# Optimization experiments

Measured on AMD Instinct MI355X. Metric: run time of the kernel, lower is better.

Reference implementation:

```python
import jax, jax.numpy as jnp
import numpy as np

B, D, L = 2, 256, 512
NL, DS, DC = 2, 16, 4  # n_layers per direction, d_state, d_conv (mamba defaults, expand=2)


def _group_params(key, dm, n):
    di = 2 * dm                 # d_inner = expand * d_model
    r = -(-dm // 16)            # dt_rank = ceil(d_model / 16)
    ks = jax.random.split(key, 6)
    return dict(
        in_w=jax.random.normal(ks[0], (n, 2 * di, dm)) * 0.02,
        conv_w=jax.random.normal(ks[1], (n, di, DC)) * 0.1,
        conv_b=jnp.zeros((n, di)),
        xproj_w=jax.random.normal(ks[2], (n, r + 2 * DS, di)) * 0.02,
        dt_w=jax.random.normal(ks[3], (n, di, r)) * 0.02,
        dt_b=jax.random.normal(ks[4], (n, di)) * 0.02,
        A_log=jnp.log(jnp.tile(jnp.arange(1, DS + 1, dtype=jnp.float32), (n, di, 1))),
        D=jnp.ones((n, di)),
        out_w=jax.random.normal(ks[5], (n, dm, di)) * 0.02,
    )


def setup_inputs() -> dict:
    key = jax.random.key(0)
    kx, ka, kb = jax.random.split(key, 3)
    inp = {"x": jax.random.normal(kx, (B, D, L), dtype=jnp.float32)}
    # group a: seq-direction mambas (d_model = L); group b: channel-direction (d_model = D)
    for pfx, dm, k in (("a_", L, ka), ("b_", D, kb)):
        for name, v in _group_params(k, dm, NL).items():
            inp[pfx + name] = v
    return inp


def _mamba_layer(x, in_w, conv_w, conv_b, xproj_w, dt_w, dt_b, A_log, Dp, out_w):
    b, l, dm = x.shape
    di = in_w.shape[0] // 2
    r = dt_w.shape[1]
    xz = jnp.einsum('bld,ed->ble', x, in_w)            # (b,l,2*di)
    xi, z = jnp.split(xz, 2, axis=-1)
    # causal depthwise conv along the sequence dim
    xc = jax.lax.conv_general_dilated(
        xi.transpose(0, 2, 1), conv_w[:, None, :], (1,), [(DC - 1, 0)],
        feature_group_count=di, dimension_numbers=('NCH', 'OIH', 'NCH'))
    xi = jax.nn.silu((xc + conv_b[None, :, None]).transpose(0, 2, 1))   # (b,l,di)
    x_dbl = jnp.einsum('bld,ed->ble', xi, xproj_w)
    dt, Bm, Cm = jnp.split(x_dbl, [r, r + DS], axis=-1)
    dt = jax.nn.softplus(jnp.einsum('blr,dr->bld', dt, dt_w) + dt_b)    # (b,l,di)
    A = -jnp.exp(A_log)                                                 # (di,DS)
    dA = jnp.exp(dt[..., None] * A)                                     # (b,l,di,DS)
    dBu = dt[..., None] * Bm[:, :, None, :] * xi[..., None]             # (b,l,di,DS)

    def step(h, inp):
        dA_t, dBu_t, C_t = inp
        h = dA_t * h + dBu_t
        return h, jnp.einsum('bds,bs->bd', h, C_t)

    h0 = jnp.zeros((b, di, DS), x.dtype)
    _, ys = jax.lax.scan(step, h0, (dA.transpose(1, 0, 2, 3),
                                    dBu.transpose(1, 0, 2, 3),
                                    Cm.transpose(1, 0, 2)))
    y = ys.transpose(1, 0, 2) + Dp * xi
    y = y * jax.nn.silu(z)
    return jnp.einsum('bld,od->blo', y, out_w)


def _stack(x, p):
    for k in range(NL):
        x = _mamba_layer(x, p['in_w'][k], p['conv_w'][k], p['conv_b'][k],
                         p['xproj_w'][k], p['dt_w'][k], p['dt_b'][k],
                         p['A_log'][k], p['D'][k], p['out_w'][k])
    return x


def reference(x, a_in_w, a_conv_w, a_conv_b, a_xproj_w, a_dt_w, a_dt_b, a_A_log, a_D, a_out_w,
              b_in_w, b_conv_w, b_conv_b, b_xproj_w, b_dt_w, b_dt_b, b_A_log, b_D, b_out_w):
    pa = dict(in_w=a_in_w, conv_w=a_conv_w, conv_b=a_conv_b, xproj_w=a_xproj_w,
              dt_w=a_dt_w, dt_b=a_dt_b, A_log=a_A_log, D=a_D, out_w=a_out_w)
    pb = dict(in_w=b_in_w, conv_w=b_conv_w, conv_b=b_conv_b, xproj_w=b_xproj_w,
              dt_w=b_dt_w, dt_b=b_dt_b, A_log=b_A_log, D=b_D, out_w=b_out_w)
    h = _stack(x, pa)                                        # mamba over last dim L on (B,D,L)
    h = _stack(h.transpose(0, 2, 1), pb).transpose(0, 2, 1)  # mamba over channel dim D
    return x + h
```

## Files before the change

kernel.cpp:

```cpp
#include <hip/hip_runtime.h>
#include <cstdint>

typedef float f32x4 __attribute__((ext_vector_type(4)));
typedef __bf16 bf16x8 __attribute__((ext_vector_type(8)));
typedef __bf16 bf16x4 __attribute__((ext_vector_type(4)));

#define SCAN_TC 32

struct CvtP {
    const float* cs[5]; __bf16* cd[5]; int cn[5]; int nvec;
    const float* xpb; __bf16* xpb_d;
};

__global__ __launch_bounds__(256)
void cvt_all(CvtP p)
{
    const int idx = blockIdx.x * 256 + threadIdx.x;
    if (idx < p.nvec) {
        int off = idx * 4, sgm = 0;
        while (off >= p.cn[sgm]) { off -= p.cn[sgm]; ++sgm; }
        f32x4 v = *(const f32x4*)(p.cs[sgm] + off);
        bf16x4 o;
#pragma unroll
        for (int j = 0; j < 4; ++j) o[j] = (__bf16)v[j];
        *(bf16x4*)(p.cd[sgm] + off) = o;
    } else {
        const int i = idx - p.nvec;
        if (i < 2 * 64 * 512) {
            const int c = i & 511, r = (i >> 9) & 63, l = i >> 15;
            float v = (r < 48) ? p.xpb[((size_t)l * 48 + r) * 512 + c] : 0.f;
            p.xpb_d[i] = (__bf16)v;
        }
    }
}

__global__ __launch_bounds__(256)
void gemm_f32A(const float* __restrict__ A, const __bf16* __restrict__ W,
               float* __restrict__ C, int M, int N, int K)
{
    __shared__ __bf16 sA[64 * 64];
    __shared__ __bf16 sW[64 * 64];
    const int tid = threadIdx.x;
    const int bm = blockIdx.y * 64, bn = blockIdx.x * 64;
    const int lane = tid & 63, wv = tid >> 6;
    const int m_off = (wv & 1) * 32, n_off = (wv >> 1) * 32;
    const int fr = lane & 15, fq = lane >> 4;
    f32x4 acc[2][2] = {};

    for (int k0 = 0; k0 < K; k0 += 64) {
#pragma unroll
        for (int i = 0; i < 2; ++i) {
            const int cid = i * 256 + tid;
            const int row = cid >> 3, kc = cid & 7;
            const int slot = kc ^ (row & 7);
            const float* sa = A + (size_t)(bm + row) * K + k0 + kc * 8;
            f32x4 v0 = *(const f32x4*)sa;
            f32x4 v1 = *(const f32x4*)(sa + 4);
            bf16x8 ab;
#pragma unroll
            for (int j = 0; j < 4; ++j) { ab[j] = (__bf16)v0[j]; ab[4 + j] = (__bf16)v1[j]; }
            *(bf16x8*)&sA[row * 64 + slot * 8] = ab;
            *(bf16x8*)&sW[row * 64 + slot * 8] =
                *(const bf16x8*)(W + (size_t)(bn + row) * K + k0 + kc * 8);
        }
        __syncthreads();
#pragma unroll
        for (int ks = 0; ks < 2; ++ks) {
            const int kc = ks * 4 + fq;
            const int r0 = m_off + fr, r1 = m_off + 16 + fr;
            const int c0 = n_off + fr, c1 = n_off + 16 + fr;
            bf16x8 a0 = *(const bf16x8*)&sA[r0 * 64 + (kc ^ (r0 & 7)) * 8];
            bf16x8 a1 = *(const bf16x8*)&sA[r1 * 64 + (kc ^ (r1 & 7)) * 8];
            bf16x8 b0 = *(const bf16x8*)&sW[c0 * 64 + (kc ^ (c0 & 7)) * 8];
            bf16x8 b1 = *(const bf16x8*)&sW[c1 * 64 + (kc ^ (c1 & 7)) * 8];
            acc[0][0] = __builtin_amdgcn_mfma_f32_16x16x32_bf16(a0, b0, acc[0][0], 0, 0, 0);
            acc[0][1] = __builtin_amdgcn_mfma_f32_16x16x32_bf16(a0, b1, acc[0][1], 0, 0, 0);
            acc[1][0] = __builtin_amdgcn_mfma_f32_16x16x32_bf16(a1, b0, acc[1][0], 0, 0, 0);
            acc[1][1] = __builtin_amdgcn_mfma_f32_16x16x32_bf16(a1, b1, acc[1][1], 0, 0, 0);
        }
        __syncthreads();
    }
#pragma unroll
    for (int i = 0; i < 2; ++i)
#pragma unroll
        for (int j = 0; j < 2; ++j)
#pragma unroll
            for (int r = 0; r < 4; ++r)
                C[(size_t)(bm + m_off + i * 16 + fq * 4 + r) * N
                  + bn + n_off + j * 16 + fr] = acc[i][j][r];
}

__global__ __launch_bounds__(256)
void gemm_b16A(const __bf16* __restrict__ A, const __bf16* __restrict__ W,
               float* __restrict__ C, int M, int N, int K)
{
    __shared__ __bf16 sA[64 * 64];
    __shared__ __bf16 sW[64 * 64];
    const int tid = threadIdx.x;
    const int bm = blockIdx.y * 64, bn = blockIdx.x * 64;
    const int lane = tid & 63, wv = tid >> 6;
    const int m_off = (wv & 1) * 32, n_off = (wv >> 1) * 32;
    const int fr = lane & 15, fq = lane >> 4;
    f32x4 acc[2][2] = {};

    for (int k0 = 0; k0 < K; k0 += 64) {
#pragma unroll
        for (int i = 0; i < 2; ++i) {
            const int cid = i * 256 + tid;
            const int row = cid >> 3, kc = cid & 7;
            const int slot = kc ^ (row & 7);
            *(bf16x8*)&sA[row * 64 + slot * 8] =
                *(const bf16x8*)(A + (size_t)(bm + row) * K + k0 + kc * 8);
            *(bf16x8*)&sW[row * 64 + slot * 8] =
                *(const bf16x8*)(W + (size_t)(bn + row) * K + k0 + kc * 8);
        }
        __syncthreads();
#pragma unroll
        for (int ks = 0; ks < 2; ++ks) {
            const int kc = ks * 4 + fq;
            const int r0 = m_off + fr, r1 = m_off + 16 + fr;
            const int c0 = n_off + fr, c1 = n_off + 16 + fr;
            bf16x8 a0 = *(const bf16x8*)&sA[r0 * 64 + (kc ^ (r0 & 7)) * 8];
            bf16x8 a1 = *(const bf16x8*)&sA[r1 * 64 + (kc ^ (r1 & 7)) * 8];
            bf16x8 b0 = *(const bf16x8*)&sW[c0 * 64 + (kc ^ (c0 & 7)) * 8];
            bf16x8 b1 = *(const bf16x8*)&sW[c1 * 64 + (kc ^ (c1 & 7)) * 8];
            acc[0][0] = __builtin_amdgcn_mfma_f32_16x16x32_bf16(a0, b0, acc[0][0], 0, 0, 0);
            acc[0][1] = __builtin_amdgcn_mfma_f32_16x16x32_bf16(a0, b1, acc[0][1], 0, 0, 0);
            acc[1][0] = __builtin_amdgcn_mfma_f32_16x16x32_bf16(a1, b0, acc[1][0], 0, 0, 0);
            acc[1][1] = __builtin_amdgcn_mfma_f32_16x16x32_bf16(a1, b1, acc[1][1], 0, 0, 0);
        }
        __syncthreads();
    }
#pragma unroll
    for (int i = 0; i < 2; ++i)
#pragma unroll
        for (int j = 0; j < 2; ++j)
#pragma unroll
            for (int r = 0; r < 4; ++r)
                C[(size_t)(bm + m_off + i * 16 + fq * 4 + r) * N
                  + bn + n_off + j * 16 + fr] = acc[i][j][r];
}

__global__ __launch_bounds__(256)
void gemm_out(const __bf16* __restrict__ A, const __bf16* __restrict__ W,
              void* __restrict__ dst, const float* __restrict__ resid,
              int M, int N, int K, int Lb, int mode)
{
    const int tid = threadIdx.x, lane = tid & 63, wv = tid >> 6;
    const int bm = blockIdx.y * 32 + (wv & 1) * 16;
    const int bn = blockIdx.x * 32 + (wv >> 1) * 16;
    const int fr = lane & 15, fq = lane >> 4;
    const __bf16* arow = A + (size_t)(bm + fr) * K + fq * 8;
    const __bf16* brow = W + (size_t)(bn + fr) * K + fq * 8;
    f32x4 acc0 = {}, acc1 = {};
#pragma unroll 2
    for (int k0 = 0; k0 < K; k0 += 64) {
        bf16x8 a0 = *(const bf16x8*)(arow + k0);
        bf16x8 b0 = *(const bf16x8*)(brow + k0);
        bf16x8 a1 = *(const bf16x8*)(arow + k0 + 32);
        bf16x8 b1 = *(const bf16x8*)(brow + k0 + 32);
        acc0 = __builtin_amdgcn_mfma_f32_16x16x32_bf16(a0, b0, acc0, 0, 0, 0);
        acc1 = __builtin_amdgcn_mfma_f32_16x16x32_bf16(a1, b1, acc1, 0, 0, 0);
    }
    f32x4 acc = acc0 + acc1;
    const int col = bn + fr;
#pragma unroll
    for (int r = 0; r < 4; ++r) {
        const int gm = bm + fq * 4 + r;
        if (mode == 0) {
            ((__bf16*)dst)[(size_t)gm * N + col] = (__bf16)acc[r];
        } else {
            const int b = gm / Lb, t = gm - b * Lb;
            const size_t o = ((size_t)(b * N + col)) * Lb + t;
            if (mode == 1) ((__bf16*)dst)[o] = (__bf16)acc[r];
            else ((float*)dst)[o] = acc[r] + resid[o];
        }
    }
}

__global__ __launch_bounds__(256)
void fused_xp(const float* __restrict__ xz, const float* __restrict__ conv_w,
              const float* __restrict__ conv_b, const __bf16* __restrict__ W,
              float* __restrict__ xi_out, float* __restrict__ pbuf,
              int M, int K, int KC, int Lb)
{
    __shared__ __bf16 sA[64 * 64];
    __shared__ __bf16 sW[64 * 64];
    const int tid = threadIdx.x;
    const int bm = blockIdx.y * 64;
    const int kb = blockIdx.x * KC;
    const int lane = tid & 63, wv = tid >> 6;
    const int m_off = (wv & 1) * 32, n_off = (wv >> 1) * 32;
    const int fr = lane & 15, fq = lane >> 4;
    const int DI = K;
    const int b = bm / Lb;
    const int tbase = bm - b * Lb;
    f32x4 acc[2][2] = {};

    for (int k0 = kb; k0 < kb + KC; k0 += 64) {
#pragma unroll
        for (int i = 0; i < 2; ++i) {
            const int cid = i * 256 + tid;
            const int row = cid >> 3, kc = cid & 7;
            const int slot = kc ^ (row & 7);
            const int d0 = k0 + kc * 8;
            const int t = tbase + row;
            f32x4 a0 = *(const f32x4*)&conv_b[d0];
            f32x4 a1 = *(const f32x4*)&conv_b[d0 + 4];
            f32x4 wc[8];
#pragma unroll
            for (int cch = 0; cch < 8; ++cch)
                wc[cch] = *(const f32x4*)&conv_w[(size_t)(d0 + cch) * 4];
#pragma unroll
            for (int jj = 0; jj < 4; ++jj) {
                const int tt = t - 3 + jj;
                if (tt >= 0) {
                    const float* src = xz + (size_t)(b * Lb + tt) * (2 * DI) + d0;
                    f32x4 v0 = *(const f32x4*)src;
                    f32x4 v1 = *(const f32x4*)(src + 4);
#pragma unroll
                    for (int cch = 0; cch < 4; ++cch) {
                        a0[cch] = fmaf(wc[cch][jj], v0[cch], a0[cch]);
                        a1[cch] = fmaf(wc[4 + cch][jj], v1[cch], a1[cch]);
                    }
                }
            }
            f32x4 r0v, r1v; bf16x8 ab;
#pragma unroll
            for (int cch = 0; cch < 4; ++cch) {
                const float u0 = a0[cch], u1 = a1[cch];
                const float s0 = u0 / (1.f + __expf(-u0));
                const float s1 = u1 / (1.f + __expf(-u1));
                r0v[cch] = s0; r1v[cch] = s1;
                ab[cch] = (__bf16)s0; ab[4 + cch] = (__bf16)s1;
            }
            const size_t mrow = (size_t)(bm + row);
            *(f32x4*)&xi_out[mrow * DI + d0] = r0v;
            *(f32x4*)&xi_out[mrow * DI + d0 + 4] = r1v;
            *(bf16x8*)&sA[row * 64 + slot * 8] = ab;
            *(bf16x8*)&sW[row * 64 + slot * 8] =
                *(const bf16x8*)(W + (size_t)row * K + k0 + kc * 8);
        }
        __syncthreads();
#pragma unroll
        for (int ksu = 0; ksu < 2; ++ksu) {
            const int kc = ksu * 4 + fq;
            const int r0 = m_off + fr, r1 = m_off + 16 + fr;
            const int c0 = n_off + fr, c1 = n_off + 16 + fr;
            bf16x8 a0 = *(const bf16x8*)&sA[r0 * 64 + (kc ^ (r0 & 7)) * 8];
            bf16x8 a1 = *(const bf16x8*)&sA[r1 * 64 + (kc ^ (r1 & 7)) * 8];
            bf16x8 b0 = *(const bf16x8*)&sW[c0 * 64 + (kc ^ (c0 & 7)) * 8];
            bf16x8 b1 = *(const bf16x8*)&sW[c1 * 64 + (kc ^ (c1 & 7)) * 8];
            acc[0][0] = __builtin_amdgcn_mfma_f32_16x16x32_bf16(a0, b0, acc[0][0], 0, 0, 0);
            acc[0][1] = __builtin_amdgcn_mfma_f32_16x16x32_bf16(a0, b1, acc[0][1], 0, 0, 0);
            acc[1][0] = __builtin_amdgcn_mfma_f32_16x16x32_bf16(a1, b0, acc[1][0], 0, 0, 0);
            acc[1][1] = __builtin_amdgcn_mfma_f32_16x16x32_bf16(a1, b1, acc[1][1], 0, 0, 0);
        }
        __syncthreads();
    }
    float* out = pbuf + (size_t)blockIdx.x * M * 64;
#pragma unroll
    for (int i = 0; i < 2; ++i)
#pragma unroll
        for (int jj = 0; jj < 2; ++jj)
#pragma unroll
            for (int r = 0; r < 4; ++r)
                out[(size_t)(bm + m_off + i * 16 + fq * 4 + r) * 64
                    + n_off + jj * 16 + fr] = acc[i][jj][r];
}

__global__ __launch_bounds__(256)
void xp_reduce(const float* __restrict__ pbuf, float* __restrict__ xdbl,
               int total, int KS)
{
    const int idx = (blockIdx.x * 256 + threadIdx.x) * 4;
    if (idx >= total) return;
    f32x4 s = {0.f, 0.f, 0.f, 0.f};
    for (int ks = 0; ks < KS; ++ks)
        s += *(const f32x4*)(pbuf + (size_t)ks * total + idx);
    *(f32x4*)(xdbl + idx) = s;
}

__global__ __launch_bounds__(256)
void scan_p1(const float* __restrict__ xi, const float* __restrict__ xdbl,
             const float* __restrict__ dtw, const float* __restrict__ dtb,
             const float* __restrict__ A_log,
             float* __restrict__ wsA, float* __restrict__ wsB,
             int Bb, int Lb, int DI, int R, int P)
{
    __shared__ float s_xd[SCAN_TC][64];
    __shared__ float s_dt[SCAN_TC][16];
    __shared__ float s_xi[SCAN_TC][16];
    __shared__ float s_w[16 * 33];
    __shared__ float s_db[16];
    const int tid = threadIdx.x;
    const int s = tid & 15, dl = tid >> 4;
    const int nDB = DI / 16;
    const int cpb = P * nDB;
    const int b = blockIdx.x / cpb;
    const int rem = blockIdx.x % cpb;
    const int c = rem / nDB;
    const int d0 = (rem % nDB) * 16;
    const int d = d0 + dl;
    const size_t rowbase = (size_t)b * Lb + (size_t)c * SCAN_TC;

    for (int idx = tid; idx < 16 * R; idx += 256)
        s_w[(idx / R) * 33 + (idx % R)] = dtw[(size_t)(d0 + idx / R) * R + idx % R];
    if (tid < 16) s_db[tid] = dtb[d0 + tid];
#pragma unroll
    for (int i = 0; i < 8; ++i) {
        const int e = i * 256 + tid;
        const int tt = e >> 6, col = e & 63;
        s_xd[tt][col] = xdbl[(rowbase + tt) * 64 + col];
    }
#pragma unroll
    for (int i = 0; i < 2; ++i) {
        const int e = i * 256 + tid;
        const int tt = e >> 4, dd = e & 15;
        s_xi[tt][dd] = xi[(rowbase + tt) * DI + d0 + dd];
    }
    __syncthreads();
#pragma unroll
    for (int i = 0; i < 2; ++i) {
        const int pr = i * 256 + tid;
        const int tt = pr >> 4, dd = pr & 15;
        float v = s_db[dd];
        for (int r = 0; r < R; ++r) v = fmaf(s_xd[tt][r], s_w[dd * 33 + r], v);
        s_dt[tt][dd] = fmaxf(v, 0.f) + log1pf(__expf(-fabsf(v)));
    }
    __syncthreads();
    const float A = -__expf(A_log[(size_t)d * 16 + s]);
    float h = 0.f, sdt = 0.f;
#pragma unroll 4
    for (int t = 0; t < SCAN_TC; ++t) {
        const float dtv = s_dt[t][dl];
        const float xv  = s_xi[t][dl];
        const float Bv  = s_xd[t][R + s];
        h = fmaf(__expf(dtv * A), h, dtv * Bv * xv);
        sdt += dtv;
    }
    const size_t o = ((size_t)(b * P + c) * DI + d) * 16 + s;
    wsA[o] = __expf(sdt * A);
    wsB[o] = h;
}

__global__ __launch_bounds__(256)
void scan_p23(const float* __restrict__ xi, const float* __restrict__ xdbl,
              const float* __restrict__ xz,
              const float* __restrict__ dtw, const float* __restrict__ dtb,
              const float* __restrict__ A_log, const float* __restrict__ Dp,
              const float* __restrict__ wsA, const float* __restrict__ wsB,
              __bf16* __restrict__ y,
              int Bb, int Lb, int DI, int R, int P)
{
    __shared__ float s_xd[SCAN_TC][64];
    __shared__ float s_dt[SCAN_TC][16];
    __shared__ float s_xi[SCAN_TC][16];
    __shared__ float s_z [SCAN_TC][16];
    __shared__ float s_w[16 * 33];
    __shared__ float s_db[16];
    const int tid = threadIdx.x;
    const int s = tid & 15, dl = tid >> 4;
    const int nDB = DI / 16;
    const int cpb = P * nDB;
    const int b = blockIdx.x / cpb;
    const int rem = blockIdx.x % cpb;
    const int c = rem / nDB;
    const int d0 = (rem % nDB) * 16;
    const int d = d0 + dl;
    const size_t rowbase = (size_t)b * Lb + (size_t)c * SCAN_TC;

    for (int idx = tid; idx < 16 * R; idx += 256)
        s_w[(idx / R) * 33 + (idx % R)] = dtw[(size_t)(d0 + idx / R) * R + idx % R];
    if (tid < 16) s_db[tid] = dtb[d0 + tid];
#pragma unroll
    for (int i = 0; i < 8; ++i) {
        const int e = i * 256 + tid;
        const int tt = e >> 6, col = e & 63;
        s_xd[tt][col] = xdbl[(rowbase + tt) * 64 + col];
    }
#pragma unroll
    for (int i = 0; i < 2; ++i) {
        const int e = i * 256 + tid;
        const int tt = e >> 4, dd = e & 15;
        s_xi[tt][dd] = xi[(rowbase + tt) * DI + d0 + dd];
        s_z [tt][dd] = xz[(rowbase + tt) * (size_t)(2 * DI) + DI + d0 + dd];
    }
    __syncthreads();
#pragma unroll
    for (int i = 0; i < 2; ++i) {
        const int pr = i * 256 + tid;
        const int tt = pr >> 4, dd = pr & 15;
        float v = s_db[dd];
        for (int r = 0; r < R; ++r) v = fmaf(s_xd[tt][r], s_w[dd * 33 + r], v);
        s_dt[tt][dd] = fmaxf(v, 0.f) + log1pf(__expf(-fabsf(v)));
    }
    __syncthreads();
    const float A = -__expf(A_log[(size_t)d * 16 + s]);
    const float Dv = Dp[d];

    float h = 0.f;
    for (int cc = 0; cc < c; ++cc) {
        const size_t oc = ((size_t)(b * P + cc) * DI + d) * 16 + s;
        h = fmaf(wsA[oc], h, wsB[oc]);
    }
#pragma unroll 2
    for (int t = 0; t < SCAN_TC; ++t) {
        const float dtv = s_dt[t][dl];
        const float xv  = s_xi[t][dl];
        const float Bv  = s_xd[t][R + s];
        const float Cv  = s_xd[t][R + 16 + s];
        h = fmaf(__expf(dtv * A), h, dtv * Bv * xv);
        float p = h * Cv;
        p += __shfl_xor(p, 1, 16);
        p += __shfl_xor(p, 2, 16);
        p += __shfl_xor(p, 4, 16);
        p += __shfl_xor(p, 8, 16);
        if (s == 0) {
            const float zv = s_z[t][dl];
            const float sig = __fdividef(zv, 1.f + __expf(-zv));
            y[(rowbase + t) * DI + d] = (__bf16)((p + Dv * xv) * sig);
        }
    }
}

extern "C" void kernel_launch(void* const* d_in, const int* in_sizes, int n_in,
                              void* d_out, int out_size, void* d_ws, size_t ws_size,
                              hipStream_t stream)
{
    const float* x       = (const float*)d_in[0];
    const float* a_in_w  = (const float*)d_in[1];
    const float* a_convw = (const float*)d_in[2];
    const float* a_convb = (const float*)d_in[3];
    const float* a_xproj = (const float*)d_in[4];
    const float* a_dtw   = (const float*)d_in[5];
    const float* a_dtb   = (const float*)d_in[6];
    const float* a_Alog  = (const float*)d_in[7];
    const float* a_Dp    = (const float*)d_in[8];
    const float* a_outw  = (const float*)d_in[9];
    const float* b_in_w  = (const float*)d_in[10];
    const float* b_convw = (const float*)d_in[11];
    const float* b_convb = (const float*)d_in[12];
    const float* b_xproj = (const float*)d_in[13];
    const float* b_dtw   = (const float*)d_in[14];
    const float* b_dtb   = (const float*)d_in[15];
    const float* b_Alog  = (const float*)d_in[16];
    const float* b_Dp    = (const float*)d_in[17];
    const float* b_outw  = (const float*)d_in[18];

    float* ws = (float*)d_ws;
    float* buf_xz   = ws;
    float* buf_xi   = buf_xz + 1048576;
    float* buf_xd   = buf_xi + 524288;
    float* buf_pk   = buf_xd + 65536;
    float* buf_wsA  = buf_pk + 524288;
    float* buf_wsB  = buf_wsA + 262144;
    __bf16* wb       = (__bf16*)(buf_wsB + 262144);
    __bf16* wb_a_in  = wb;
    __bf16* wb_a_out = wb_a_in + 2097152;
    __bf16* wb_b_in  = wb_a_out + 1048576;
    __bf16* wb_b_out = wb_b_in + 524288;
    __bf16* wb_xp_a  = wb_b_out + 262144;
    __bf16* wb_xp_b  = wb_xp_a + 131072;
    __bf16* buf_xb   = wb_xp_b + 65536;
    __bf16* buf_x2b  = buf_xb + 262144;
    __bf16* buf_yb   = buf_x2b + 262144;

    {
        CvtP cp;
        cp.cs[0] = a_in_w;  cp.cd[0] = wb_a_in;  cp.cn[0] = 2097152;
        cp.cs[1] = a_outw;  cp.cd[1] = wb_a_out; cp.cn[1] = 1048576;
        cp.cs[2] = b_in_w;  cp.cd[2] = wb_b_in;  cp.cn[2] = 524288;
        cp.cs[3] = b_outw;  cp.cd[3] = wb_b_out; cp.cn[3] = 262144;
        cp.cs[4] = a_xproj; cp.cd[4] = wb_xp_a;  cp.cn[4] = 131072;
        cp.nvec = (2097152 + 1048576 + 524288 + 262144 + 131072) / 4;
        cp.xpb = b_xproj; cp.xpb_d = wb_xp_b;
        const int nthr = cp.nvec + 2 * 64 * 512;
        cvt_all<<<(nthr + 255) / 256, 256, 0, stream>>>(cp);
    }

    for (int k = 0; k < 2; ++k) {
        const int Bb = 2, Lb = 256, DM = 512, DI = 1024, R = 32, P = 8, KS = 16;
        const int M = Bb * Lb;
        if (k == 0)
            gemm_f32A<<<dim3(2 * DI / 64, M / 64), 256, 0, stream>>>(
                x, wb_a_in + (size_t)k * 2 * DI * DM, buf_xz, M, 2 * DI, DM);
        else
            gemm_b16A<<<dim3(2 * DI / 64, M / 64), 256, 0, stream>>>(
                buf_xb, wb_a_in + (size_t)k * 2 * DI * DM, buf_xz, M, 2 * DI, DM);
        fused_xp<<<dim3(KS, M / 64), 256, 0, stream>>>(
            buf_xz, a_convw + (size_t)k * DI * 4, a_convb + (size_t)k * DI,
            wb_xp_a + (size_t)k * 64 * DI, buf_xi, buf_pk, M, DI, DI / KS, Lb);
        xp_reduce<<<(M * 64 / 4 + 255) / 256, 256, 0, stream>>>(
            buf_pk, buf_xd, M * 64, KS);
        scan_p1<<<Bb * P * DI / 16, 256, 0, stream>>>(
            buf_xi, buf_xd, a_dtw + (size_t)k * DI * R, a_dtb + (size_t)k * DI,
            a_Alog + (size_t)k * DI * 16, buf_wsA, buf_wsB, Bb, Lb, DI, R, P);
        scan_p23<<<Bb * P * DI / 16, 256, 0, stream>>>(
            buf_xi, buf_xd, buf_xz, a_dtw + (size_t)k * DI * R, a_dtb + (size_t)k * DI,
            a_Alog + (size_t)k * DI * 16, a_Dp + (size_t)k * DI,
            buf_wsA, buf_wsB, buf_yb, Bb, Lb, DI, R, P);
        if (k == 0)
            gemm_out<<<dim3(DM / 32, M / 32), 256, 0, stream>>>(
                buf_yb, wb_a_out + (size_t)k * DM * DI, buf_xb, nullptr,
                M, DM, DI, Lb, 0);
        else
            gemm_out<<<dim3(DM / 32, M / 32), 256, 0, stream>>>(
                buf_yb, wb_a_out + (size_t)k * DM * DI, buf_x2b, nullptr,
                M, DM, DI, Lb, 1);
    }

    for (int k = 0; k < 2; ++k) {
        const int Bb = 2, Lb = 512, DM = 256, DI = 512, R = 16, P = 16, KS = 8;
        const int M = Bb * Lb;
        const __bf16* src = (k == 0) ? buf_x2b : buf_xb;
        gemm_b16A<<<dim3(2 * DI / 64, M / 64), 256, 0, stream>>>(
            src, wb_b_in + (size_t)k * 2 * DI * DM, buf_xz, M, 2 * DI, DM);
        fused_xp<<<dim3(KS, M / 64), 256, 0, stream>>>(
            buf_xz, b_convw + (size_t)k * DI * 4, b_convb + (size_t)k * DI,
            wb_xp_b + (size_t)k * 64 * DI, buf_xi, buf_pk, M, DI, DI / KS, Lb);
        xp_reduce<<<(M * 64 / 4 + 255) / 256, 256, 0, stream>>>(
            buf_pk, buf_xd, M * 64, KS);
        scan_p1<<<Bb * P * DI / 16, 256, 0, stream>>>(
            buf_xi, buf_xd, b_dtw + (size_t)k * DI * R, b_dtb + (size_t)k * DI,
            b_Alog + (size_t)k * DI * 16, buf_wsA, buf_wsB, Bb, Lb, DI, R, P);
        scan_p23<<<Bb * P * DI / 16, 256, 0, stream>>>(
            buf_xi, buf_xd, buf_xz, b_dtw + (size_t)k * DI * R, b_dtb + (size_t)k * DI,
            b_Alog + (size_t)k * DI * 16, b_Dp + (size_t)k * DI,
            buf_wsA, buf_wsB, buf_yb, Bb, Lb, DI, R, P);
        if (k == 0)
            gemm_out<<<dim3(DM / 32, M / 32), 256, 0, stream>>>(
                buf_yb, wb_b_out + (size_t)k * DM * DI, buf_xb, nullptr,
                M, DM, DI, Lb, 0);
        else
            gemm_out<<<dim3(DM / 32, M / 32), 256, 0, stream>>>(
                buf_yb, wb_b_out + (size_t)k * DM * DI, d_out, x,
                M, DM, DI, Lb, 2);
    }
}
```

Before: 218.9 us.

## Fuse chunked scan passes into one kernel with in-block carry propagation

Replaces the two-kernel chunked selective scan (chunk summaries written to global workspace, then a second kernel that re-reduces all prior chunk summaries serially) with one kernel per (batch, 8-channel group). Each block of 512 threads covers all chunks of the sequence in four chunk groups, keeps chunk summaries in shared memory, runs a short serial prefix over chunks, then recomputes each chunk with its carried state. This removes a launch per layer, the global workspace round trip and the quadratic carry loop. In exchange the grid is much smaller (256 or 128 blocks), each block loops over chunks sequentially, and dt and the x_dbl tiles are recomputed or reloaded in both passes.

```diff
diff --git a/kernel.cpp b/kernel.cpp
--- a/kernel.cpp
+++ b/kernel.cpp
@@ -6,6 +6,7 @@
 typedef __bf16 bf16x4 __attribute__((ext_vector_type(4)));
 
 #define SCAN_TC 32
+#define NG 4
 
 struct CvtP {
     const float* cs[5]; __bf16* cd[5]; int cn[5]; int nvec;
@@ -281,145 +282,123 @@
     *(f32x4*)(xdbl + idx) = s;
 }
 
-__global__ __launch_bounds__(256)
-void scan_p1(const float* __restrict__ xi, const float* __restrict__ xdbl,
-             const float* __restrict__ dtw, const float* __restrict__ dtb,
-             const float* __restrict__ A_log,
-             float* __restrict__ wsA, float* __restrict__ wsB,
-             int Bb, int Lb, int DI, int R, int P)
-{
-    __shared__ float s_xd[SCAN_TC][64];
-    __shared__ float s_dt[SCAN_TC][16];
-    __shared__ float s_xi[SCAN_TC][16];
-    __shared__ float s_w[16 * 33];
-    __shared__ float s_db[16];
+__global__ __launch_bounds__(512)
+void scan_fused(const float* __restrict__ xi, const float* __restrict__ xdbl,
+                const float* __restrict__ xz,
+                const float* __restrict__ dtw, const float* __restrict__ dtb,
+                const float* __restrict__ A_log, const float* __restrict__ Dp,
+                __bf16* __restrict__ y, int Bb, int Lb, int DI, int R, int P)
+{
+    __shared__ float s_xd[NG][SCAN_TC][64];
+    __shared__ float s_xi[NG][SCAN_TC][8];
+    __shared__ float s_z [NG][SCAN_TC][8];
+    __shared__ float s_dt[NG][SCAN_TC][8];
+    __shared__ float s_w[8][33];
+    __shared__ float s_db[8];
+    __shared__ float sumA[16][128];
+    __shared__ float sumB[16][128];
+
     const int tid = threadIdx.x;
-    const int s = tid & 15, dl = tid >> 4;
-    const int nDB = DI / 16;
-    const int cpb = P * nDB;
-    const int b = blockIdx.x / cpb;
-    const int rem = blockIdx.x % cpb;
-    const int c = rem / nDB;
-    const int d0 = (rem % nDB) * 16;
+    const int cg = tid >> 7;
+    const int lt = tid & 127;
+    const int s = lt & 15, dl = lt >> 4;
+    const int nD8 = DI >> 3;
+    const int b = blockIdx.x / nD8;
+    const int d0 = (blockIdx.x % nD8) * 8;
     const int d = d0 + dl;
-    const size_t rowbase = (size_t)b * Lb + (size_t)c * SCAN_TC;
-
-    for (int idx = tid; idx < 16 * R; idx += 256)
-        s_w[(idx / R) * 33 + (idx % R)] = dtw[(size_t)(d0 + idx / R) * R + idx % R];
-    if (tid < 16) s_db[tid] = dtb[d0 + tid];
-#pragma unroll
-    for (int i = 0; i < 8; ++i) {
-        const int e = i * 256 + tid;
-        const int tt = e >> 6, col = e & 63;
-        s_xd[tt][col] = xdbl[(rowbase + tt) * 64 + col];
-    }
-#pragma unroll
-    for (int i = 0; i < 2; ++i) {
-        const int e = i * 256 + tid;
-        const int tt = e >> 4, dd = e & 15;
-        s_xi[tt][dd] = xi[(rowbase + tt) * DI + d0 + dd];
-    }
-    __syncthreads();
-#pragma unroll
-    for (int i = 0; i < 2; ++i) {
-        const int pr = i * 256 + tid;
-        const int tt = pr >> 4, dd = pr & 15;
-        float v = s_db[dd];
-        for (int r = 0; r < R; ++r) v = fmaf(s_xd[tt][r], s_w[dd * 33 + r], v);
-        s_dt[tt][dd] = fmaxf(v, 0.f) + log1pf(__expf(-fabsf(v)));
-    }
-    __syncthreads();
-    const float A = -__expf(A_log[(size_t)d * 16 + s]);
-    float h = 0.f, sdt = 0.f;
-#pragma unroll 4
-    for (int t = 0; t < SCAN_TC; ++t) {
-        const float dtv = s_dt[t][dl];
-        const float xv  = s_xi[t][dl];
-        const float Bv  = s_xd[t][R + s];
-        h = fmaf(__expf(dtv * A), h, dtv * Bv * xv);
-        sdt += dtv;
-    }
-    const size_t o = ((size_t)(b * P + c) * DI + d) * 16 + s;
-    wsA[o] = __expf(sdt * A);
-    wsB[o] = h;
-}
-
-__global__ __launch_bounds__(256)
-void scan_p23(const float* __restrict__ xi, const float* __restrict__ xdbl,
-              const float* __restrict__ xz,
-              const float* __restrict__ dtw, const float* __restrict__ dtb,
-              const float* __restrict__ A_log, const float* __restrict__ Dp,
-              const float* __restrict__ wsA, const float* __restrict__ wsB,
-              __bf16* __restrict__ y,
-              int Bb, int Lb, int DI, int R, int P)
-{
-    __shared__ float s_xd[SCAN_TC][64];
-    __shared__ float s_dt[SCAN_TC][16];
-    __shared__ float s_xi[SCAN_TC][16];
-    __shared__ float s_z [SCAN_TC][16];
-    __shared__ float s_w[16 * 33];
-    __shared__ float s_db[16];
-    const int tid = threadIdx.x;
-    const int s = tid & 15, dl = tid >> 4;
-    const int nDB = DI / 16;
-    const int cpb = P * nDB;
-    const int b = blockIdx.x / cpb;
-    const int rem = blockIdx.x % cpb;
-    const int c = rem / nDB;
-    const int d0 = (rem % nDB) * 16;
-    const int d = d0 + dl;
-    const size_t rowbase = (size_t)b * Lb + (size_t)c * SCAN_TC;
-
-    for (int idx = tid; idx < 16 * R; idx += 256)
-        s_w[(idx / R) * 33 + (idx % R)] = dtw[(size_t)(d0 + idx / R) * R + idx % R];
-    if (tid < 16) s_db[tid] = dtb[d0 + tid];
-#pragma unroll
-    for (int i = 0; i < 8; ++i) {
-        const int e = i * 256 + tid;
-        const int tt = e >> 6, col = e & 63;
-        s_xd[tt][col] = xdbl[(rowbase + tt) * 64 + col];
-    }
-#pragma unroll
-    for (int i = 0; i < 2; ++i) {
-        const int e = i * 256 + tid;
-        const int tt = e >> 4, dd = e & 15;
-        s_xi[tt][dd] = xi[(rowbase + tt) * DI + d0 + dd];
-        s_z [tt][dd] = xz[(rowbase + tt) * (size_t)(2 * DI) + DI + d0 + dd];
-    }
-    __syncthreads();
-#pragma unroll
-    for (int i = 0; i < 2; ++i) {
-        const int pr = i * 256 + tid;
-        const int tt = pr >> 4, dd = pr & 15;
-        float v = s_db[dd];
-        for (int r = 0; r < R; ++r) v = fmaf(s_xd[tt][r], s_w[dd * 33 + r], v);
-        s_dt[tt][dd] = fmaxf(v, 0.f) + log1pf(__expf(-fabsf(v)));
-    }
-    __syncthreads();
+    const int CPG = P / NG;
+
+    for (int idx = tid; idx < 8 * R; idx += 512)
+        s_w[idx / R][idx % R] = dtw[(size_t)(d0 + idx / R) * R + idx % R];
+    if (tid < 8) s_db[tid] = dtb[d0 + tid];
     const float A = -__expf(A_log[(size_t)d * 16 + s]);
     const float Dv = Dp[d];
 
-    float h = 0.f;
-    for (int cc = 0; cc < c; ++cc) {
-        const size_t oc = ((size_t)(b * P + cc) * DI + d) * 16 + s;
-        h = fmaf(wsA[oc], h, wsB[oc]);
-    }
+    for (int i = 0; i < CPG; ++i) {
+        const int c = cg + i * NG;
+        const size_t rowbase = (size_t)b * Lb + (size_t)c * SCAN_TC;
+        __syncthreads();
+        {
+            const f32x4* src = (const f32x4*)(xdbl + rowbase * 64);
+            f32x4* dst = (f32x4*)&s_xd[cg][0][0];
+            for (int e = lt; e < 512; e += 128) dst[e] = src[e];
+        }
+        for (int e = lt; e < 256; e += 128) {
+            const int tt = e >> 3, dd = e & 7;
+            s_xi[cg][tt][dd] = xi[(rowbase + tt) * DI + d0 + dd];
+        }
+        __syncthreads();
+        for (int e = lt; e < 256; e += 128) {
+            const int tt = e >> 3, dd = e & 7;
+            float v = s_db[dd];
+            for (int r = 0; r < R; ++r) v = fmaf(s_xd[cg][tt][r], s_w[dd][r], v);
+            s_dt[cg][tt][dd] = fmaxf(v, 0.f) + log1pf(__expf(-fabsf(v)));
+        }
+        __syncthreads();
+        float h = 0.f, sdt = 0.f;
+#pragma unroll 4
+        for (int t = 0; t < SCAN_TC; ++t) {
+            const float dtv = s_dt[cg][t][dl];
+            const float xv  = s_xi[cg][t][dl];
+            const float Bv  = s_xd[cg][t][R + s];
+            h = fmaf(__expf(dtv * A), h, dtv * Bv * xv);
+            sdt += dtv;
+        }
+        sumA[c][lt] = __expf(sdt * A);
+        sumB[c][lt] = h;
+    }
+    __syncthreads();
+
+    if (tid < 128) {
+        float h = 0.f;
+        for (int c = 0; c < P; ++c) {
+            const float a = sumA[c][tid], bv = sumB[c][tid];
+            sumA[c][tid] = h;
+            h = fmaf(a, h, bv);
+        }
+    }
+    __syncthreads();
+
+    for (int i = 0; i < CPG; ++i) {
+        const int c = cg + i * NG;
+        const size_t rowbase = (size_t)b * Lb + (size_t)c * SCAN_TC;
+        float h = sumA[c][lt];
+        __syncthreads();
+        {
+            const f32x4* src = (const f32x4*)(xdbl + rowbase * 64);
+            f32x4* dst = (f32x4*)&s_xd[cg][0][0];
+            for (int e = lt; e < 512; e += 128) dst[e] = src[e];
+        }
+        for (int e = lt; e < 256; e += 128) {
+            const int tt = e >> 3, dd = e & 7;
+            s_xi[cg][tt][dd] = xi[(rowbase + tt) * DI + d0 + dd];
+            s_z [cg][tt][dd] = xz[(rowbase + tt) * (size_t)(2 * DI) + DI + d0 + dd];
+        }
+        __syncthreads();
+        for (int e = lt; e < 256; e += 128) {
+            const int tt = e >> 3, dd = e & 7;
+            float v = s_db[dd];
+            for (int r = 0; r < R; ++r) v = fmaf(s_xd[cg][tt][r], s_w[dd][r], v);
+            s_dt[cg][tt][dd] = fmaxf(v, 0.f) + log1pf(__expf(-fabsf(v)));
+        }
+        __syncthreads();
 #pragma unroll 2
-    for (int t = 0; t < SCAN_TC; ++t) {
-        const float dtv = s_dt[t][dl];
-        const float xv  = s_xi[t][dl];
-        const float Bv  = s_xd[t][R + s];
-        const float Cv  = s_xd[t][R + 16 + s];
-        h = fmaf(__expf(dtv * A), h, dtv * Bv * xv);
-        float p = h * Cv;
-        p += __shfl_xor(p, 1, 16);
-        p += __shfl_xor(p, 2, 16);
-        p += __shfl_xor(p, 4, 16);
-        p += __shfl_xor(p, 8, 16);
-        if (s == 0) {
-            const float zv = s_z[t][dl];
-            const float sig = __fdividef(zv, 1.f + __expf(-zv));
-            y[(rowbase + t) * DI + d] = (__bf16)((p + Dv * xv) * sig);
+        for (int t = 0; t < SCAN_TC; ++t) {
+            const float dtv = s_dt[cg][t][dl];
+            const float xv  = s_xi[cg][t][dl];
+            const float Bv  = s_xd[cg][t][R + s];
+            const float Cv  = s_xd[cg][t][R + 16 + s];
+            h = fmaf(__expf(dtv * A), h, dtv * Bv * xv);
+            float p = h * Cv;
+            p += __shfl_xor(p, 1, 16);
+            p += __shfl_xor(p, 2, 16);
+            p += __shfl_xor(p, 4, 16);
+            p += __shfl_xor(p, 8, 16);
+            if (s == 0) {
+                const float zv = s_z[cg][t][dl];
+                const float sig = __fdividef(zv, 1.f + __expf(-zv));
+                y[(rowbase + t) * DI + d] = (__bf16)((p + Dv * xv) * sig);
+            }
         }
     }
 }
@@ -453,9 +432,7 @@
     float* buf_xi   = buf_xz + 1048576;
     float* buf_xd   = buf_xi + 524288;
     float* buf_pk   = buf_xd + 65536;
-    float* buf_wsA  = buf_pk + 524288;
-    float* buf_wsB  = buf_wsA + 262144;
-    __bf16* wb       = (__bf16*)(buf_wsB + 262144);
+    __bf16* wb       = (__bf16*)(buf_pk + 524288);
     __bf16* wb_a_in  = wb;
     __bf16* wb_a_out = wb_a_in + 2097152;
     __bf16* wb_b_in  = wb_a_out + 1048576;
@@ -493,13 +470,10 @@
             wb_xp_a + (size_t)k * 64 * DI, buf_xi, buf_pk, M, DI, DI / KS, Lb);
         xp_reduce<<<(M * 64 / 4 + 255) / 256, 256, 0, stream>>>(
             buf_pk, buf_xd, M * 64, KS);
-        scan_p1<<<Bb * P * DI / 16, 256, 0, stream>>>(
-            buf_xi, buf_xd, a_dtw + (size_t)k * DI * R, a_dtb + (size_t)k * DI,
-            a_Alog + (size_t)k * DI * 16, buf_wsA, buf_wsB, Bb, Lb, DI, R, P);
-        scan_p23<<<Bb * P * DI / 16, 256, 0, stream>>>(
+        scan_fused<<<Bb * DI / 8, 512, 0, stream>>>(
             buf_xi, buf_xd, buf_xz, a_dtw + (size_t)k * DI * R, a_dtb + (size_t)k * DI,
             a_Alog + (size_t)k * DI * 16, a_Dp + (size_t)k * DI,
-            buf_wsA, buf_wsB, buf_yb, Bb, Lb, DI, R, P);
+            buf_yb, Bb, Lb, DI, R, P);
         if (k == 0)
             gemm_out<<<dim3(DM / 32, M / 32), 256, 0, stream>>>(
                 buf_yb, wb_a_out + (size_t)k * DM * DI, buf_xb, nullptr,
@@ -521,13 +495,10 @@
             wb_xp_b + (size_t)k * 64 * DI, buf_xi, buf_pk, M, DI, DI / KS, Lb);
         xp_reduce<<<(M * 64 / 4 + 255) / 256, 256, 0, stream>>>(
             buf_pk, buf_xd, M * 64, KS);
-        scan_p1<<<Bb * P * DI / 16, 256, 0, stream>>>(
-            buf_xi, buf_xd, b_dtw + (size_t)k * DI * R, b_dtb + (size_t)k * DI,
-            b_Alog + (size_t)k * DI * 16, buf_wsA, buf_wsB, Bb, Lb, DI, R, P);
-        scan_p23<<<Bb * P * DI / 16, 256, 0, stream>>>(
+        scan_fused<<<Bb * DI / 8, 512, 0, stream>>>(
             buf_xi, buf_xd, buf_xz, b_dtw + (size_t)k * DI * R, b_dtb + (size_t)k * DI,
             b_Alog + (size_t)k * DI * 16, b_Dp + (size_t)k * DI,
-            buf_wsA, buf_wsB, buf_yb, Bb, Lb, DI, R, P);
+            buf_yb, Bb, Lb, DI, R, P);
         if (k == 0)
             gemm_out<<<dim3(DM / 32, M / 32), 256, 0, stream>>>(
                 buf_yb, wb_b_out + (size_t)k * DM * DI, buf_xb, nullptr,
```

Result: slower. 335.2 us (+53.1%).
